# Kernel optimization log

Measured on AMD Instinct MI355X. Metric: run time of the kernel, lower is better.

The kernel has to match this reference:

```python
import jax, jax.numpy as jnp
import numpy as np

B, S, D, H = 2, 2048, 1024, 16
DK = D // H  # 64
THETA = 10000.0


def _rope_tables(max_seq_len, d_k, theta):
    dim_idx = jnp.arange(0, d_k // 2, dtype=jnp.float32)
    freqs = 1.0 / theta ** (2.0 * dim_idx / d_k)
    pos = jnp.arange(0, max_seq_len, dtype=jnp.float32)
    ang = jnp.outer(pos, freqs)  # [S, d_k//2]
    return jnp.sin(ang), jnp.cos(ang)


def setup_inputs() -> dict:
    key = jax.random.key(0)
    ks = jax.random.split(key, 5)
    scale = 0.02
    x = jax.random.normal(ks[0], (B, S, D), dtype=jnp.float32)
    w_q = jax.random.normal(ks[1], (D, D), dtype=jnp.float32) * scale
    w_k = jax.random.normal(ks[2], (D, D), dtype=jnp.float32) * scale
    w_v = jax.random.normal(ks[3], (D, D), dtype=jnp.float32) * scale
    w_o = jax.random.normal(ks[4], (D, D), dtype=jnp.float32) * scale
    sin_tab, cos_tab = _rope_tables(S, DK, THETA)
    token_positions = jnp.broadcast_to(jnp.arange(S, dtype=jnp.int32), (B, S))
    return {"x": x, "w_q": w_q, "w_k": w_k, "w_v": w_v, "w_o": w_o,
            "sin_tab": sin_tab, "cos_tab": cos_tab,
            "token_positions": token_positions}


def _apply_rope(t, sin, cos):
    # t: [B, H, S, DK]; sin/cos: [B, 1, S, DK//2]
    t_even = t[..., 0::2]
    t_odd = t[..., 1::2]
    r_even = cos * t_even - sin * t_odd
    r_odd = sin * t_even + cos * t_odd
    # re-interleave even/odd back into last dim
    out = jnp.stack([r_even, r_odd], axis=-1)  # [B,H,S,DK//2,2]
    return out.reshape(t.shape)


def reference(x, w_q, w_k, w_v, w_o, sin_tab, cos_tab, token_positions):
    b, s, d = x.shape
    q = (x @ w_q.T).reshape(b, s, H, DK).transpose(0, 2, 1, 3)  # [B,H,S,DK]
    k = (x @ w_k.T).reshape(b, s, H, DK).transpose(0, 2, 1, 3)
    v = (x @ w_v.T).reshape(b, s, H, DK).transpose(0, 2, 1, 3)

    sin = sin_tab[token_positions][:, None, :, :]  # [B,1,S,DK//2]
    cos = cos_tab[token_positions][:, None, :, :]
    q = _apply_rope(q, sin, cos)
    k = _apply_rope(k, sin, cos)

    scores = jnp.einsum('bhqd,bhkd->bhqk', q, k) / jnp.sqrt(jnp.float32(DK))
    causal = jnp.tril(jnp.ones((s, s), dtype=bool))  # keep lower triangle
    scores = jnp.where(causal, scores, -jnp.inf)
    probs = jax.nn.softmax(scores, axis=-1)
    attn = jnp.einsum('bhqk,bhkd->bhqd', probs, v)
    attn = attn.transpose(0, 2, 1, 3).reshape(b, s, d)
    return attn @ w_o.T
```

## Files before the change

### kernel.cpp

```cpp
#include <hip/hip_runtime.h>
#include <hip/hip_bf16.h>
#include <cstdint>

#define B_ 2
#define S_ 2048
#define D_ 1024
#define H_ 16
#define DK_ 64
#define HALF_ 32

typedef short bf16x8 __attribute__((ext_vector_type(8)));
typedef float f32x4  __attribute__((ext_vector_type(4)));
typedef unsigned int u32;

static __device__ __forceinline__ unsigned short bfbits(float f) {
    __hip_bfloat16 h = __float2bfloat16(f);
    unsigned short u; __builtin_memcpy(&u, &h, 2); return u;
}
static __device__ __forceinline__ unsigned pack2bf(float a, float b) {
    return (unsigned)bfbits(a) | ((unsigned)bfbits(b) << 16);
}

static __device__ __forceinline__ void gload_lds16(const void* g, void* l) {
    __builtin_amdgcn_global_load_lds(
        (const __attribute__((address_space(1))) u32*)(uintptr_t)g,
        (__attribute__((address_space(3))) u32*)(uintptr_t)l,
        16, 0, 0);
}

__global__ __launch_bounds__(256) void to_bf16_kernel(
    const float* __restrict__ x,
    const float* __restrict__ wq, const float* __restrict__ wk,
    const float* __restrict__ wv, const float* __restrict__ wo,
    const float* __restrict__ sin_tab, const float* __restrict__ cos_tab,
    __hip_bfloat16* __restrict__ xb,
    __hip_bfloat16* __restrict__ wqb, __hip_bfloat16* __restrict__ wkb,
    __hip_bfloat16* __restrict__ wvb, __hip_bfloat16* __restrict__ wob,
    float2* __restrict__ sctab)
{
    const int seg = blockIdx.y;
    if (seg == 8) {
        if (blockIdx.x >= 64) return;
        size_t i = ((size_t)blockIdx.x * 256 + threadIdx.x) * 4;
        float4 c = *reinterpret_cast<const float4*>(cos_tab + i);
        float4 s = *reinterpret_cast<const float4*>(sin_tab + i);
        float4* dst = reinterpret_cast<float4*>(sctab + i);
        dst[0] = make_float4(c.x, s.x, c.y, s.y);
        dst[1] = make_float4(c.z, s.z, c.w, s.w);
        return;
    }
    const float* src;
    __hip_bfloat16* dst;
    size_t off = 0;
    if (seg < 4)       { src = x;  dst = xb;  off = (size_t)seg << 20; }
    else if (seg == 4) { src = wq; dst = wqb; }
    else if (seg == 5) { src = wk; dst = wkb; }
    else if (seg == 6) { src = wv; dst = wvb; }
    else               { src = wo; dst = wob; }
    size_t i = off + ((size_t)blockIdx.x * 256 + threadIdx.x) * 4;
    float4 v = *reinterpret_cast<const float4*>(src + i);
    ushort4 u = make_ushort4(bfbits(v.x), bfbits(v.y), bfbits(v.z), bfbits(v.w));
    *reinterpret_cast<ushort4*>(dst + i) = u;
}

template<int MODE>
__global__ __launch_bounds__(256) void mfma_gemm_kernel(
    const __hip_bfloat16* __restrict__ A,
    const __hip_bfloat16* __restrict__ Wq, const __hip_bfloat16* __restrict__ Wk,
    const __hip_bfloat16* __restrict__ Wv,
    __hip_bfloat16* __restrict__ out_q, __hip_bfloat16* __restrict__ out_k,
    __hip_bfloat16* __restrict__ out_v,
    float* __restrict__ out_f32,
    const float2* __restrict__ sctab,
    const int* __restrict__ tpos)
{
    constexpr int K = 1024;
    const int which = (MODE == 0) ? blockIdx.z : 3;
    const __hip_bfloat16* __restrict__ W =
        (MODE == 1) ? Wq : (which == 0 ? Wq : which == 1 ? Wk : Wv);

    __shared__ __align__(16) unsigned char As[2][128 * 4 * 16];
    __shared__ __align__(16) unsigned char Bs[2][128 * 4 * 16];

    const int tid = threadIdx.x;
    const int wid = tid >> 6;
    const int l   = tid & 63;
    const int g   = l >> 4;
    const int i16 = l & 15;
    const int wr  = wid >> 1, wc = wid & 1;

    const int wg   = blockIdx.x;
    const int tile = (wg & 7) * 32 + (wg >> 3);
    const int row0 = (tile >> 3) * 128;
    const int col0 = (tile & 7) * 128;

    const __hip_bfloat16* Abase = A + (size_t)row0 * K;
    const __hip_bfloat16* Wbase = W + (size_t)col0 * K;

    f32x4 acc[4][4];
    const f32x4 zero = {0.f, 0.f, 0.f, 0.f};
    #pragma unroll
    for (int mi = 0; mi < 4; ++mi)
        #pragma unroll
        for (int ni = 0; ni < 4; ++ni) acc[mi][ni] = zero;

    int a_off[4], b_off[4];
    #pragma unroll
    for (int f = 0; f < 4; ++f) {
        int ra = wr * 64 + f * 16 + i16;
        a_off[f] = (ra * 4 + (g ^ ((ra >> 1) & 3))) * 16;
        int rb = wc * 64 + f * 16 + i16;
        b_off[f] = (rb * 4 + (g ^ ((rb >> 1) & 3))) * 16;
    }

    int st_goff[2], st_loff[2];
    #pragma unroll
    for (int it = 0; it < 2; ++it) {
        int c = it * 256 + wid * 64 + l;
        int row = c >> 2;
        int kc = (c & 3) ^ ((row >> 1) & 3);
        st_goff[it] = row * K + kc * 8;
        st_loff[it] = (it * 256 + wid * 64) * 16;
    }

    #pragma unroll
    for (int it = 0; it < 2; ++it) {
        gload_lds16(Abase + st_goff[it], &As[0][0] + st_loff[it]);
        gload_lds16(Wbase + st_goff[it], &Bs[0][0] + st_loff[it]);
    }
    __syncthreads();

    for (int t = 0; t < K / 32; ++t) {
        const int cur = t & 1;
        if (t + 1 < K / 32) {
            const int k1 = (t + 1) * 32;
            #pragma unroll
            for (int it = 0; it < 2; ++it) {
                gload_lds16(Abase + k1 + st_goff[it], &As[cur ^ 1][0] + st_loff[it]);
                gload_lds16(Wbase + k1 + st_goff[it], &Bs[cur ^ 1][0] + st_loff[it]);
            }
        }
        bf16x8 af[4], bfr[4];
        #pragma unroll
        for (int f = 0; f < 4; ++f) {
            af[f]  = *reinterpret_cast<const bf16x8*>(&As[cur][0] + a_off[f]);
            bfr[f] = *reinterpret_cast<const bf16x8*>(&Bs[cur][0] + b_off[f]);
        }
        #pragma unroll
        for (int mi = 0; mi < 4; ++mi)
            #pragma unroll
            for (int ni = 0; ni < 4; ++ni)
                acc[mi][ni] = __builtin_amdgcn_mfma_f32_16x16x32_bf16(
                    af[mi], bfr[ni], acc[mi][ni], 0, 0, 0);
        __syncthreads();
    }

    if (MODE == 0) {
        __hip_bfloat16* __restrict__ outp =
            which == 0 ? out_q : which == 1 ? out_k : out_v;
        const int head = (col0 >> 6) + wc;
        #pragma unroll
        for (int mi = 0; mi < 4; ++mi) {
            #pragma unroll
            for (int r = 0; r < 4; ++r) {
                const int gi = row0 + wr * 64 + mi * 16 + g * 4 + r;
                const int b_ = gi >> 11;
                const int s_ = gi & (S_ - 1);
                const int pos = tpos[gi];
                const float2* sc = sctab + pos * HALF_;
                __hip_bfloat16* orow =
                    outp + (((size_t)b_ * H_ + head) * S_ + s_) * DK_;
                #pragma unroll
                for (int ni = 0; ni < 4; ++ni) {
                    float val = acc[mi][ni][r];
                    float other = __shfl_xor(val, 1, 64);
                    const int dk = ni * 16 + i16;
                    float res;
                    if (which < 2) {
                        float2 cs = sc[ni * 8 + (i16 >> 1)];
                        res = (i16 & 1) ? fmaf(cs.y, other, cs.x * val)
                                        : (cs.x * val - cs.y * other);
                    } else {
                        res = val;
                    }
                    if (which == 0) res *= 0.180336880f;
                    orow[dk] = __float2bfloat16(res);
                }
            }
        }
    } else {
        #pragma unroll
        for (int mi = 0; mi < 4; ++mi) {
            #pragma unroll
            for (int r = 0; r < 4; ++r) {
                const int gi = row0 + wr * 64 + mi * 16 + g * 4 + r;
                float* orow = out_f32 + (size_t)gi * D_ + col0 + wc * 64;
                #pragma unroll
                for (int ni = 0; ni < 4; ++ni)
                    orow[ni * 16 + i16] = acc[mi][ni][r];
            }
        }
    }
}

__global__ __launch_bounds__(256) void flash_mfma_kernel(
    const __hip_bfloat16* __restrict__ q,
    const __hip_bfloat16* __restrict__ k,
    const __hip_bfloat16* __restrict__ v,
    __hip_bfloat16* __restrict__ attn)
{
    __shared__ __align__(16) unsigned char Ks[2][64 * 128];
    __shared__ __align__(16) unsigned char Vt[2][64 * 128];
    __shared__ __align__(16) unsigned char Ps[4][16 * 128];

    const int tid = threadIdx.x;
    const int w   = tid >> 6;
    const int l   = tid & 63;
    const int g   = l >> 4;
    const int i16 = l & 15;

    const int wgid = blockIdx.x;
    const int xcd  = wgid & 7;
    const int idx  = wgid >> 3;
    const int r_   = idx >> 5;
    const int c_   = idx & 31;
    const int bh   = xcd * 4 + r_;
    const int qsb  = (r_ & 1) ? c_ : (31 - c_);

    const size_t base = (size_t)bh * S_ * DK_;
    const __hip_bfloat16* kb_ = k + base;
    const __hip_bfloat16* vb_ = v + base;
    const int nt = qsb + 1;

    int ksrc[2], kdst[2];
    #pragma unroll
    for (int it = 0; it < 2; ++it) {
        int c = it * 256 + tid;
        int krow = c >> 3;
        int kchunk = (c & 7) ^ (krow & 7);
        ksrc[it] = krow * DK_ + kchunk * 8;
        kdst[it] = c * 16;
    }
    const int vd8_0 = w;
    const int vd8_1 = 4 + w;
    unsigned char* const pw = &Ps[w][0];

    const int qrow = qsb * 64 + w * 16 + i16;

    bf16x8 qf0, qf1;
    {
        const __hip_bfloat16* qp = q + base + (size_t)qrow * DK_ + g * 8;
        qf0 = *reinterpret_cast<const bf16x8*>(qp);
        qf1 = *reinterpret_cast<const bf16x8*>(qp + 32);
    }

    f32x4 o[4] = {};
    float m_run = -1e30f, l_run = 0.0f;

    #pragma unroll
    for (int it = 0; it < 2; ++it)
        gload_lds16(kb_ + ksrc[it], &Ks[0][0] + kdst[it]);
    {
        float4 vv0 = *reinterpret_cast<const float4*>(vb_ + l * DK_ + vd8_0 * 8);
        float4 vv1 = *reinterpret_cast<const float4*>(vb_ + l * DK_ + vd8_1 * 8);
        const unsigned short* u0 = reinterpret_cast<const unsigned short*>(&vv0);
        const unsigned short* u1 = reinterpret_cast<const unsigned short*>(&vv1);
        #pragma unroll
        for (int s = 0; s < 8; ++s) {
            int d0 = vd8_0 * 8 + s;
            *reinterpret_cast<unsigned short*>(&Vt[0][0] + d0 * 128 +
                (((l >> 3) ^ (d0 & 7)) << 4) + (l & 7) * 2) = u0[s];
            int d1 = vd8_1 * 8 + s;
            *reinterpret_cast<unsigned short*>(&Vt[0][0] + d1 * 128 +
                (((l >> 3) ^ (d1 & 7)) << 4) + (l & 7) * 2) = u1[s];
        }
    }
    __syncthreads();

    for (int t = 0; t < nt; ++t) {
        const int cur = t & 1;
        const bool pre = (t + 1 < nt);
        float4 vv0, vv1;
        if (pre) {
            const size_t toff = (size_t)(t + 1) * 64 * DK_;
            #pragma unroll
            for (int it = 0; it < 2; ++it)
                gload_lds16(kb_ + toff + ksrc[it], &Ks[cur ^ 1][0] + kdst[it]);
            vv0 = *reinterpret_cast<const float4*>(vb_ + toff + l * DK_ + vd8_0 * 8);
            vv1 = *reinterpret_cast<const float4*>(vb_ + toff + l * DK_ + vd8_1 * 8);
        }

        f32x4 s_acc[4] = {};
        __builtin_amdgcn_s_setprio(1);
        #pragma unroll
        for (int jf = 0; jf < 4; ++jf) {
            int row = jf * 16 + i16;
            bf16x8 ak0 = *reinterpret_cast<const bf16x8*>(
                &Ks[cur][0] + row * 128 + ((g ^ (row & 7)) << 4));
            s_acc[jf] = __builtin_amdgcn_mfma_f32_16x16x32_bf16(
                ak0, qf0, s_acc[jf], 0, 0, 0);
            bf16x8 ak1 = *reinterpret_cast<const bf16x8*>(
                &Ks[cur][0] + row * 128 + (((4 + g) ^ (row & 7)) << 4));
            s_acc[jf] = __builtin_amdgcn_mfma_f32_16x16x32_bf16(
                ak1, qf1, s_acc[jf], 0, 0, 0);
        }
        __builtin_amdgcn_s_setprio(0);

        if (t == nt - 1) {
            #pragma unroll
            for (int jf = 0; jf < 4; ++jf)
                #pragma unroll
                for (int r = 0; r < 4; ++r)
                    if (t * 64 + jf * 16 + g * 4 + r > qrow)
                        s_acc[jf][r] = -1e30f;
        }

        float mx0 = fmaxf(fmaxf(s_acc[0][0], s_acc[0][1]),
                          fmaxf(s_acc[0][2], s_acc[0][3]));
        float mx1 = fmaxf(fmaxf(s_acc[1][0], s_acc[1][1]),
                          fmaxf(s_acc[1][2], s_acc[1][3]));
        float mx2 = fmaxf(fmaxf(s_acc[2][0], s_acc[2][1]),
                          fmaxf(s_acc[2][2], s_acc[2][3]));
        float mx3 = fmaxf(fmaxf(s_acc[3][0], s_acc[3][1]),
                          fmaxf(s_acc[3][2], s_acc[3][3]));
        float vmax = fmaxf(fmaxf(mx0, mx1), fmaxf(mx2, mx3));

        if (!__all(vmax <= m_run + 11.5f)) {
            float rmax = fmaxf(vmax, __shfl_xor(vmax, 16, 64));
            rmax = fmaxf(rmax, __shfl_xor(rmax, 32, 64));
            float m_new = fmaxf(m_run, rmax);
            float factor = __builtin_amdgcn_exp2f(m_run - m_new);
            m_run = m_new;
            l_run *= factor;
            #pragma unroll
            for (int df = 0; df < 4; ++df)
                #pragma unroll
                for (int r = 0; r < 4; ++r)
                    o[df][r] *= factor;
        }

        float p[4][4];
        float psum = 0.0f;
        #pragma unroll
        for (int jf = 0; jf < 4; ++jf)
            #pragma unroll
            for (int r = 0; r < 4; ++r) {
                p[jf][r] = __builtin_amdgcn_exp2f(s_acc[jf][r] - m_run);
                psum += p[jf][r];
            }
        l_run += psum;

        #pragma unroll
        for (int jf = 0; jf < 4; ++jf)
            #pragma unroll
            for (int r0 = 0; r0 < 4; r0 += 2) {
                unsigned pk = pack2bf(p[jf][r0], p[jf][r0 + 1]);
                int jj = jf * 16 + g * 4 + r0;
                *reinterpret_cast<unsigned*>(pw + i16 * 128 +
                    ((jj * 2) ^ ((i16 & 7) << 4))) = pk;
            }

        __builtin_amdgcn_s_setprio(1);
        #pragma unroll
        for (int jc = 0; jc < 2; ++jc) {
            bf16x8 bp = *reinterpret_cast<const bf16x8*>(pw + i16 * 128 +
                (((jc * 4 + g) ^ (i16 & 7)) << 4));
            #pragma unroll
            for (int df = 0; df < 4; ++df) {
                int row = df * 16 + i16;
                bf16x8 av = *reinterpret_cast<const bf16x8*>(
                    &Vt[cur][0] + row * 128 +
                    (((jc * 4 + g) ^ (row & 7)) << 4));
                o[df] = __builtin_amdgcn_mfma_f32_16x16x32_bf16(
                    av, bp, o[df], 0, 0, 0);
            }
        }
        __builtin_amdgcn_s_setprio(0);

        if (pre) {
            unsigned char* vtb = &Vt[cur ^ 1][0];
            const unsigned short* u0 = reinterpret_cast<const unsigned short*>(&vv0);
            const unsigned short* u1 = reinterpret_cast<const unsigned short*>(&vv1);
            #pragma unroll
            for (int s = 0; s < 8; ++s) {
                int d0 = vd8_0 * 8 + s;
                *reinterpret_cast<unsigned short*>(vtb + d0 * 128 +
                    (((l >> 3) ^ (d0 & 7)) << 4) + (l & 7) * 2) = u0[s];
                int d1 = vd8_1 * 8 + s;
                *reinterpret_cast<unsigned short*>(vtb + d1 * 128 +
                    (((l >> 3) ^ (d1 & 7)) << 4) + (l & 7) * 2) = u1[s];
            }
        }
        __syncthreads();
    }

    float l_tot = l_run;
    l_tot += __shfl_xor(l_tot, 16, 64);
    l_tot += __shfl_xor(l_tot, 32, 64);
    const float inv_l = 1.0f / l_tot;
    const int b_ = bh >> 4, h_ = bh & 15;
    __hip_bfloat16* orow = attn + ((size_t)b_ * S_ + qrow) * D_ + h_ * 64;
    #pragma unroll
    for (int df = 0; df < 4; ++df) {
        ushort4 uo = make_ushort4(
            bfbits(o[df][0] * inv_l), bfbits(o[df][1] * inv_l),
            bfbits(o[df][2] * inv_l), bfbits(o[df][3] * inv_l));
        *reinterpret_cast<ushort4*>(orow + df * 16 + g * 4) = uo;
    }
}

extern "C" void kernel_launch(void* const* d_in, const int* in_sizes, int n_in,
                              void* d_out, int out_size, void* d_ws, size_t ws_size,
                              hipStream_t stream) {
    const float* x       = (const float*)d_in[0];
    const float* w_q     = (const float*)d_in[1];
    const float* w_k     = (const float*)d_in[2];
    const float* w_v     = (const float*)d_in[3];
    const float* w_o     = (const float*)d_in[4];
    const float* sin_tab = (const float*)d_in[5];
    const float* cos_tab = (const float*)d_in[6];
    const int*   tpos    = (const int*)d_in[7];
    float* out = (float*)d_out;

    const size_t nM  = (size_t)B_ * S_ * D_;
    const size_t nW  = (size_t)D_ * D_;
    __hip_bfloat16* xb   = (__hip_bfloat16*)d_ws;
    __hip_bfloat16* wqb  = xb  + nM;
    __hip_bfloat16* wkb  = wqb + nW;
    __hip_bfloat16* wvb  = wkb + nW;
    __hip_bfloat16* wob  = wvb + nW;
    __hip_bfloat16* q_ws = wob + nW;
    __hip_bfloat16* k_ws = q_ws + nM;
    __hip_bfloat16* v_ws = k_ws + nM;
    __hip_bfloat16* a_ws = v_ws + nM;
    float2*         sct  = (float2*)(a_ws + nM);

    to_bf16_kernel<<<dim3(1024, 9), 256, 0, stream>>>(
        x, w_q, w_k, w_v, w_o, sin_tab, cos_tab,
        xb, wqb, wkb, wvb, wob, sct);
    mfma_gemm_kernel<0><<<dim3(256, 1, 3), 256, 0, stream>>>(
        xb, wqb, wkb, wvb, q_ws, k_ws, v_ws, nullptr, sct, tpos);
    flash_mfma_kernel<<<1024, 256, 0, stream>>>(
        q_ws, k_ws, v_ws, a_ws);
    mfma_gemm_kernel<1><<<dim3(256, 1, 1), 256, 0, stream>>>(
        a_ws, wob, nullptr, nullptr, nullptr, nullptr, nullptr, out,
        sct, tpos);
}
```

Measured before the change: 122.0 us.

## Use 256x256-tile 8-wave GEMM with interleaved prefetch for QKV projection

Replaces the 128x128-tile QKV projection GEMM with a dedicated 512-thread kernel that computes 256x256 output tiles, with each wave holding a 128x64 accumulator block. It uses 64-wide K steps with XOR-swizzled LDS staging, and splits each step into four quadrants so the next tile's global-to-LDS loads interleave with the MFMA work. MFMA sections are bracketed by s_setprio. The goal is more reuse per loaded byte and better overlap of loads with compute. In exchange, each block uses much more LDS (128 KB) and more registers, and the grid shrinks to 192 blocks, which may underfill the 256 CUs.

```diff
diff --git a/kernel.cpp b/kernel.cpp
--- a/kernel.cpp
+++ b/kernel.cpp
@@ -63,21 +63,161 @@
     *reinterpret_cast<ushort4*>(dst + i) = u;
 }
 
-template<int MODE>
-__global__ __launch_bounds__(256) void mfma_gemm_kernel(
+__global__ __launch_bounds__(512) void qkv_gemm8_kernel(
     const __hip_bfloat16* __restrict__ A,
     const __hip_bfloat16* __restrict__ Wq, const __hip_bfloat16* __restrict__ Wk,
     const __hip_bfloat16* __restrict__ Wv,
     __hip_bfloat16* __restrict__ out_q, __hip_bfloat16* __restrict__ out_k,
     __hip_bfloat16* __restrict__ out_v,
-    float* __restrict__ out_f32,
     const float2* __restrict__ sctab,
     const int* __restrict__ tpos)
 {
+    constexpr int K  = 1024;
+    constexpr int NT = K / 64;
+    const int which = blockIdx.z;
+    const __hip_bfloat16* __restrict__ W =
+        which == 0 ? Wq : which == 1 ? Wk : Wv;
+    __hip_bfloat16* __restrict__ outp =
+        which == 0 ? out_q : which == 1 ? out_k : out_v;
+
+    __shared__ __align__(16) unsigned char As[2][32768];
+    __shared__ __align__(16) unsigned char Bs[2][32768];
+
+    const int tid = threadIdx.x;
+    const int w   = tid >> 6;
+    const int l   = tid & 63;
+    const int g   = l >> 4;
+    const int i16 = l & 15;
+    const int wr  = w >> 2;
+    const int wc  = w & 3;
+
+    const int bid = blockIdx.x;
+    const int rt  = (bid & 7) + ((bid >> 3) & 1) * 8;
+    const int ct  = bid >> 4;
+    const int row0 = rt * 256, col0 = ct * 256;
+
+    const __hip_bfloat16* Abase = A + (size_t)row0 * K;
+    const __hip_bfloat16* Wbase = W + (size_t)col0 * K;
+
+    int st_goff[2], st_loff[2];
+    #pragma unroll
+    for (int it = 0; it < 2; ++it) {
+        int c  = it * 512 + tid;
+        int rw = c >> 3;
+        int kc = (c & 7) ^ (rw & 7);
+        st_goff[it] = rw * K + kc * 8;
+        st_loff[it] = c * 16;
+    }
+
+    const int x7 = (i16 & 7) << 4;
+    const int ck0 = (g << 4) ^ x7;
+    const int ck1 = ((4 + g) << 4) ^ x7;
+    int arow[8], brow[4];
+    #pragma unroll
+    for (int mf = 0; mf < 8; ++mf) arow[mf] = (wr * 128 + mf * 16 + i16) * 128;
+    #pragma unroll
+    for (int nf = 0; nf < 4; ++nf) brow[nf] = (wc * 64 + nf * 16 + i16) * 128;
+
+    f32x4 acc[8][4];
+    const f32x4 zero = {0.f, 0.f, 0.f, 0.f};
+    #pragma unroll
+    for (int mf = 0; mf < 8; ++mf)
+        #pragma unroll
+        for (int nf = 0; nf < 4; ++nf) acc[mf][nf] = zero;
+
+    auto STAGE = [&](int isB, int h, int kt, int bufb) {
+        const __hip_bfloat16* gb = isB ? Wbase : Abase;
+        unsigned char* lb = (isB ? &Bs[bufb][0] : &As[bufb][0]) + h * 16384;
+        const size_t go = (size_t)(h * 128) * K + (size_t)kt * 64;
+        #pragma unroll
+        for (int it = 0; it < 2; ++it)
+            gload_lds16(gb + go + st_goff[it], lb + st_loff[it]);
+    };
+
+    auto QUAD = [&](int mh, int nh, int buf) {
+        bf16x8 af[4][2], bfv[2][2];
+        #pragma unroll
+        for (int mi = 0; mi < 4; ++mi) {
+            af[mi][0] = *reinterpret_cast<const bf16x8*>(
+                &As[buf][0] + arow[mh * 4 + mi] + ck0);
+            af[mi][1] = *reinterpret_cast<const bf16x8*>(
+                &As[buf][0] + arow[mh * 4 + mi] + ck1);
+        }
+        #pragma unroll
+        for (int ni = 0; ni < 2; ++ni) {
+            bfv[ni][0] = *reinterpret_cast<const bf16x8*>(
+                &Bs[buf][0] + brow[nh * 2 + ni] + ck0);
+            bfv[ni][1] = *reinterpret_cast<const bf16x8*>(
+                &Bs[buf][0] + brow[nh * 2 + ni] + ck1);
+        }
+        __builtin_amdgcn_s_setprio(1);
+        #pragma unroll
+        for (int mi = 0; mi < 4; ++mi)
+            #pragma unroll
+            for (int ni = 0; ni < 2; ++ni) {
+                acc[mh*4+mi][nh*2+ni] = __builtin_amdgcn_mfma_f32_16x16x32_bf16(
+                    af[mi][0], bfv[ni][0], acc[mh*4+mi][nh*2+ni], 0, 0, 0);
+                acc[mh*4+mi][nh*2+ni] = __builtin_amdgcn_mfma_f32_16x16x32_bf16(
+                    af[mi][1], bfv[ni][1], acc[mh*4+mi][nh*2+ni], 0, 0, 0);
+            }
+        __builtin_amdgcn_s_setprio(0);
+    };
+
+    STAGE(0, 0, 0, 0); STAGE(1, 0, 0, 0); STAGE(0, 1, 0, 0); STAGE(1, 1, 0, 0);
+
+    for (int T = 0; T < NT; ++T) {
+        const int buf = T & 1, nb = buf ^ 1;
+        const bool nl = (T + 1 < NT);
+        asm volatile("s_waitcnt vmcnt(0)\n\ts_barrier" ::: "memory");
+        if (nl) { STAGE(0, 0, T + 1, nb); STAGE(1, 0, T + 1, nb); }
+        QUAD(0, 0, buf);
+        if (nl) STAGE(0, 1, T + 1, nb);
+        QUAD(1, 0, buf);
+        if (nl) STAGE(1, 1, T + 1, nb);
+        QUAD(0, 1, buf);
+        QUAD(1, 1, buf);
+    }
+
+    const int head = ct * 4 + wc;
+    #pragma unroll
+    for (int mf = 0; mf < 8; ++mf) {
+        #pragma unroll
+        for (int r = 0; r < 4; ++r) {
+            const int gi = row0 + wr * 128 + mf * 16 + g * 4 + r;
+            const int b_ = gi >> 11;
+            const int s_ = gi & (S_ - 1);
+            const int pos = tpos[gi];
+            const float2* sc = sctab + pos * HALF_;
+            __hip_bfloat16* orow =
+                outp + (((size_t)b_ * H_ + head) * S_ + s_) * DK_;
+            #pragma unroll
+            for (int nf = 0; nf < 4; ++nf) {
+                float val = acc[mf][nf][r];
+                float other = __shfl_xor(val, 1, 64);
+                const int dk = nf * 16 + i16;
+                float res;
+                if (which < 2) {
+                    float2 cs = sc[nf * 8 + (i16 >> 1)];
+                    res = (i16 & 1) ? fmaf(cs.y, other, cs.x * val)
+                                    : (cs.x * val - cs.y * other);
+                } else {
+                    res = val;
+                }
+                if (which == 0) res *= 0.180336880f;
+                orow[dk] = __float2bfloat16(res);
+            }
+        }
+    }
+}
+
+template<int MODE>
+__global__ __launch_bounds__(256) void mfma_gemm_kernel(
+    const __hip_bfloat16* __restrict__ A,
+    const __hip_bfloat16* __restrict__ Wq,
+    float* __restrict__ out_f32)
+{
     constexpr int K = 1024;
-    const int which = (MODE == 0) ? blockIdx.z : 3;
-    const __hip_bfloat16* __restrict__ W =
-        (MODE == 1) ? Wq : (which == 0 ? Wq : which == 1 ? Wk : Wv);
+    const __hip_bfloat16* __restrict__ W = Wq;
 
     __shared__ __align__(16) unsigned char As[2][128 * 4 * 16];
     __shared__ __align__(16) unsigned char Bs[2][128 * 4 * 16];
@@ -155,50 +295,15 @@
         __syncthreads();
     }
 
-    if (MODE == 0) {
-        __hip_bfloat16* __restrict__ outp =
-            which == 0 ? out_q : which == 1 ? out_k : out_v;
-        const int head = (col0 >> 6) + wc;
-        #pragma unroll
-        for (int mi = 0; mi < 4; ++mi) {
-            #pragma unroll
-            for (int r = 0; r < 4; ++r) {
-                const int gi = row0 + wr * 64 + mi * 16 + g * 4 + r;
-                const int b_ = gi >> 11;
-                const int s_ = gi & (S_ - 1);
-                const int pos = tpos[gi];
-                const float2* sc = sctab + pos * HALF_;
-                __hip_bfloat16* orow =
-                    outp + (((size_t)b_ * H_ + head) * S_ + s_) * DK_;
-                #pragma unroll
-                for (int ni = 0; ni < 4; ++ni) {
-                    float val = acc[mi][ni][r];
-                    float other = __shfl_xor(val, 1, 64);
-                    const int dk = ni * 16 + i16;
-                    float res;
-                    if (which < 2) {
-                        float2 cs = sc[ni * 8 + (i16 >> 1)];
-                        res = (i16 & 1) ? fmaf(cs.y, other, cs.x * val)
-                                        : (cs.x * val - cs.y * other);
-                    } else {
-                        res = val;
-                    }
-                    if (which == 0) res *= 0.180336880f;
-                    orow[dk] = __float2bfloat16(res);
-                }
-            }
-        }
-    } else {
-        #pragma unroll
-        for (int mi = 0; mi < 4; ++mi) {
-            #pragma unroll
-            for (int r = 0; r < 4; ++r) {
-                const int gi = row0 + wr * 64 + mi * 16 + g * 4 + r;
-                float* orow = out_f32 + (size_t)gi * D_ + col0 + wc * 64;
-                #pragma unroll
-                for (int ni = 0; ni < 4; ++ni)
-                    orow[ni * 16 + i16] = acc[mi][ni][r];
-            }
+    #pragma unroll
+    for (int mi = 0; mi < 4; ++mi) {
+        #pragma unroll
+        for (int r = 0; r < 4; ++r) {
+            const int gi = row0 + wr * 64 + mi * 16 + g * 4 + r;
+            float* orow = out_f32 + (size_t)gi * D_ + col0 + wc * 64;
+            #pragma unroll
+            for (int ni = 0; ni < 4; ++ni)
+                orow[ni * 16 + i16] = acc[mi][ni][r];
         }
     }
 }
@@ -438,11 +543,10 @@
     to_bf16_kernel<<<dim3(1024, 9), 256, 0, stream>>>(
         x, w_q, w_k, w_v, w_o, sin_tab, cos_tab,
         xb, wqb, wkb, wvb, wob, sct);
-    mfma_gemm_kernel<0><<<dim3(256, 1, 3), 256, 0, stream>>>(
-        xb, wqb, wkb, wvb, q_ws, k_ws, v_ws, nullptr, sct, tpos);
+    qkv_gemm8_kernel<<<dim3(64, 1, 3), 512, 0, stream>>>(
+        xb, wqb, wkb, wvb, q_ws, k_ws, v_ws, sct, tpos);
     flash_mfma_kernel<<<1024, 256, 0, stream>>>(
         q_ws, k_ws, v_ws, a_ws);
     mfma_gemm_kernel<1><<<dim3(256, 1, 1), 256, 0, stream>>>(
-        a_ws, wob, nullptr, nullptr, nullptr, nullptr, nullptr, out,
-        sct, tpos);
-}
+        a_ws, wob, out);
+}
```

Measured after the change: 134.2 us. +10.1%, slower.

## Triple-buffer K tiles in flash attention with two-ahead async prefetch

Applied to the files above, without the earlier changes.

Adds a third LDS buffer for K. K tiles are now prefetched two iterations ahead with global_load_lds, while V keeps its double buffer. The end-of-iteration __syncthreads is replaced by s_waitcnt vmcnt(2) plus s_barrier, so the newest K prefetch can stay in flight across the barrier. This is meant to hide global-load latency for K, at the cost of 8 KB more shared memory per block, which could lower occupancy.

```diff
diff --git a/kernel.cpp b/kernel.cpp
--- a/kernel.cpp
+++ b/kernel.cpp
@@ -209,7 +209,7 @@
     const __hip_bfloat16* __restrict__ v,
     __hip_bfloat16* __restrict__ attn)
 {
-    __shared__ __align__(16) unsigned char Ks[2][64 * 128];
+    __shared__ __align__(16) unsigned char Ks[3][64 * 128];
     __shared__ __align__(16) unsigned char Vt[2][64 * 128];
     __shared__ __align__(16) unsigned char Ps[4][16 * 128];
 
@@ -260,6 +260,11 @@
     #pragma unroll
     for (int it = 0; it < 2; ++it)
         gload_lds16(kb_ + ksrc[it], &Ks[0][0] + kdst[it]);
+    if (nt > 1) {
+        #pragma unroll
+        for (int it = 0; it < 2; ++it)
+            gload_lds16(kb_ + 64 * DK_ + ksrc[it], &Ks[1][0] + kdst[it]);
+    }
     {
         float4 vv0 = *reinterpret_cast<const float4*>(vb_ + l * DK_ + vd8_0 * 8);
         float4 vv1 = *reinterpret_cast<const float4*>(vb_ + l * DK_ + vd8_1 * 8);
@@ -277,17 +282,24 @@
     }
     __syncthreads();
 
+    int kcur = 0;
+    int kst  = 2;
+
     for (int t = 0; t < nt; ++t) {
-        const int cur = t & 1;
-        const bool pre = (t + 1 < nt);
+        const int vcur = t & 1;
+        const bool preV = (t + 1 < nt);
+        const bool preK = (t + 2 < nt);
         float4 vv0, vv1;
-        if (pre) {
+        if (preV) {
             const size_t toff = (size_t)(t + 1) * 64 * DK_;
-            #pragma unroll
-            for (int it = 0; it < 2; ++it)
-                gload_lds16(kb_ + toff + ksrc[it], &Ks[cur ^ 1][0] + kdst[it]);
             vv0 = *reinterpret_cast<const float4*>(vb_ + toff + l * DK_ + vd8_0 * 8);
             vv1 = *reinterpret_cast<const float4*>(vb_ + toff + l * DK_ + vd8_1 * 8);
+        }
+        if (preK) {
+            const size_t toff = (size_t)(t + 2) * 64 * DK_;
+            #pragma unroll
+            for (int it = 0; it < 2; ++it)
+                gload_lds16(kb_ + toff + ksrc[it], &Ks[kst][0] + kdst[it]);
         }
 
         f32x4 s_acc[4] = {};
@@ -296,11 +308,11 @@
         for (int jf = 0; jf < 4; ++jf) {
             int row = jf * 16 + i16;
             bf16x8 ak0 = *reinterpret_cast<const bf16x8*>(
-                &Ks[cur][0] + row * 128 + ((g ^ (row & 7)) << 4));
+                &Ks[kcur][0] + row * 128 + ((g ^ (row & 7)) << 4));
             s_acc[jf] = __builtin_amdgcn_mfma_f32_16x16x32_bf16(
                 ak0, qf0, s_acc[jf], 0, 0, 0);
             bf16x8 ak1 = *reinterpret_cast<const bf16x8*>(
-                &Ks[cur][0] + row * 128 + (((4 + g) ^ (row & 7)) << 4));
+                &Ks[kcur][0] + row * 128 + (((4 + g) ^ (row & 7)) << 4));
             s_acc[jf] = __builtin_amdgcn_mfma_f32_16x16x32_bf16(
                 ak1, qf1, s_acc[jf], 0, 0, 0);
         }
@@ -369,7 +381,7 @@
             for (int df = 0; df < 4; ++df) {
                 int row = df * 16 + i16;
                 bf16x8 av = *reinterpret_cast<const bf16x8*>(
-                    &Vt[cur][0] + row * 128 +
+                    &Vt[vcur][0] + row * 128 +
                     (((jc * 4 + g) ^ (row & 7)) << 4));
                 o[df] = __builtin_amdgcn_mfma_f32_16x16x32_bf16(
                     av, bp, o[df], 0, 0, 0);
@@ -377,8 +389,8 @@
         }
         __builtin_amdgcn_s_setprio(0);
 
-        if (pre) {
-            unsigned char* vtb = &Vt[cur ^ 1][0];
+        if (preV) {
+            unsigned char* vtb = &Vt[vcur ^ 1][0];
             const unsigned short* u0 = reinterpret_cast<const unsigned short*>(&vv0);
             const unsigned short* u1 = reinterpret_cast<const unsigned short*>(&vv1);
             #pragma unroll
@@ -391,7 +403,11 @@
                     (((l >> 3) ^ (d1 & 7)) << 4) + (l & 7) * 2) = u1[s];
             }
         }
-        __syncthreads();
+        asm volatile("s_waitcnt vmcnt(2) lgkmcnt(0)\n\ts_barrier" ::: "memory");
+        __builtin_amdgcn_sched_barrier(0);
+
+        kcur = (kcur == 2) ? 0 : kcur + 1;
+        kst  = (kst  == 2) ? 0 : kst  + 1;
     }
 
     float l_tot = l_run;
```

After: 134.6 us. 10.4% more time.

## Split long causal query blocks across two workgroups and merge partial softmax results

Applied to the files above, without the earlier changes.

Query blocks 16-31, the ones with the most key tiles, are now each split into two workgroups that cover half the key range. Each half writes unnormalized bf16 partial outputs plus running max and sum to workspace, and a new merge kernel combines them into the attention output. This shortens the longest-running workgroups and evens out load across the 1536 launched workgroups. The cost is an extra kernel launch, extra global traffic for the partials, and bf16 rounding of unnormalized partial outputs.

```diff
diff --git a/kernel.cpp b/kernel.cpp
--- a/kernel.cpp
+++ b/kernel.cpp
@@ -16,6 +16,9 @@
 static __device__ __forceinline__ unsigned short bfbits(float f) {
     __hip_bfloat16 h = __float2bfloat16(f);
     unsigned short u; __builtin_memcpy(&u, &h, 2); return u;
+}
+static __device__ __forceinline__ float bf2f(unsigned short u) {
+    unsigned v = (unsigned)u << 16; float f; __builtin_memcpy(&f, &v, 4); return f;
 }
 static __device__ __forceinline__ unsigned pack2bf(float a, float b) {
     return (unsigned)bfbits(a) | ((unsigned)bfbits(b) << 16);
@@ -207,7 +210,9 @@
     const __hip_bfloat16* __restrict__ q,
     const __hip_bfloat16* __restrict__ k,
     const __hip_bfloat16* __restrict__ v,
-    __hip_bfloat16* __restrict__ attn)
+    __hip_bfloat16* __restrict__ attn,
+    __hip_bfloat16* __restrict__ opart,
+    float2* __restrict__ mlpart)
 {
     __shared__ __align__(16) unsigned char Ks[2][64 * 128];
     __shared__ __align__(16) unsigned char Vt[2][64 * 128];
@@ -222,15 +227,28 @@
     const int wgid = blockIdx.x;
     const int xcd  = wgid & 7;
     const int idx  = wgid >> 3;
-    const int r_   = idx >> 5;
-    const int c_   = idx & 31;
-    const int bh   = xcd * 4 + r_;
-    const int qsb  = (r_ & 1) ? c_ : (31 - c_);
+    const int bh   = xcd * 4 + (idx & 3);
+    const int j    = idx >> 2;
+    int qsb, t0, t1, part;
+    bool split;
+    if (j < 32) {
+        split = true;
+        qsb  = 31 - (j >> 1);
+        part = j & 1;
+        int h = (qsb + 1) >> 1;
+        t0 = part ? h : 0;
+        t1 = part ? (qsb + 1) : h;
+    } else {
+        split = false;
+        qsb  = 47 - j;
+        part = 0;
+        t0 = 0;
+        t1 = qsb + 1;
+    }
 
     const size_t base = (size_t)bh * S_ * DK_;
     const __hip_bfloat16* kb_ = k + base;
     const __hip_bfloat16* vb_ = v + base;
-    const int nt = qsb + 1;
 
     int ksrc[2], kdst[2];
     #pragma unroll
@@ -257,12 +275,13 @@
     f32x4 o[4] = {};
     float m_run = -1e30f, l_run = 0.0f;
 
-    #pragma unroll
-    for (int it = 0; it < 2; ++it)
-        gload_lds16(kb_ + ksrc[it], &Ks[0][0] + kdst[it]);
     {
-        float4 vv0 = *reinterpret_cast<const float4*>(vb_ + l * DK_ + vd8_0 * 8);
-        float4 vv1 = *reinterpret_cast<const float4*>(vb_ + l * DK_ + vd8_1 * 8);
+        const size_t toff = (size_t)t0 * 64 * DK_;
+        #pragma unroll
+        for (int it = 0; it < 2; ++it)
+            gload_lds16(kb_ + toff + ksrc[it], &Ks[0][0] + kdst[it]);
+        float4 vv0 = *reinterpret_cast<const float4*>(vb_ + toff + l * DK_ + vd8_0 * 8);
+        float4 vv1 = *reinterpret_cast<const float4*>(vb_ + toff + l * DK_ + vd8_1 * 8);
         const unsigned short* u0 = reinterpret_cast<const unsigned short*>(&vv0);
         const unsigned short* u1 = reinterpret_cast<const unsigned short*>(&vv1);
         #pragma unroll
@@ -277,9 +296,9 @@
     }
     __syncthreads();
 
-    for (int t = 0; t < nt; ++t) {
-        const int cur = t & 1;
-        const bool pre = (t + 1 < nt);
+    for (int t = t0; t < t1; ++t) {
+        const int cur = (t - t0) & 1;
+        const bool pre = (t + 1 < t1);
         float4 vv0, vv1;
         if (pre) {
             const size_t toff = (size_t)(t + 1) * 64 * DK_;
@@ -306,7 +325,7 @@
         }
         __builtin_amdgcn_s_setprio(0);
 
-        if (t == nt - 1) {
+        if (t == qsb) {
             #pragma unroll
             for (int jf = 0; jf < 4; ++jf)
                 #pragma unroll
@@ -397,16 +416,70 @@
     float l_tot = l_run;
     l_tot += __shfl_xor(l_tot, 16, 64);
     l_tot += __shfl_xor(l_tot, 32, 64);
-    const float inv_l = 1.0f / l_tot;
+
+    if (!split) {
+        const float inv_l = 1.0f / l_tot;
+        const int b_ = bh >> 4, h_ = bh & 15;
+        __hip_bfloat16* orow = attn + ((size_t)b_ * S_ + qrow) * D_ + h_ * 64;
+        #pragma unroll
+        for (int df = 0; df < 4; ++df) {
+            ushort4 uo = make_ushort4(
+                bfbits(o[df][0] * inv_l), bfbits(o[df][1] * inv_l),
+                bfbits(o[df][2] * inv_l), bfbits(o[df][3] * inv_l));
+            *reinterpret_cast<ushort4*>(orow + df * 16 + g * 4) = uo;
+        }
+    } else {
+        const int p_ = (bh * 16 + (qsb - 16)) * 2 + part;
+        const int rloc = w * 16 + i16;
+        if (g == 0) mlpart[p_ * 64 + rloc] = make_float2(m_run, l_tot);
+        __hip_bfloat16* orow = opart + ((size_t)p_ * 64 + rloc) * 64;
+        #pragma unroll
+        for (int df = 0; df < 4; ++df) {
+            ushort4 uo = make_ushort4(
+                bfbits(o[df][0]), bfbits(o[df][1]),
+                bfbits(o[df][2]), bfbits(o[df][3]));
+            *reinterpret_cast<ushort4*>(orow + df * 16 + g * 4) = uo;
+        }
+    }
+}
+
+__global__ __launch_bounds__(256) void merge_kernel(
+    const __hip_bfloat16* __restrict__ opart,
+    const float2* __restrict__ mlpart,
+    __hip_bfloat16* __restrict__ attn)
+{
+    const int u = blockIdx.x * 256 + threadIdx.x;
+    const int row = u >> 4;
+    const int dk0 = (u & 15) * 4;
+    const int bh = row >> 10;
+    const int rem = row & 1023;
+    const int qsb16 = rem >> 6;
+    const int r64 = rem & 63;
+    const int p0 = (bh * 16 + qsb16) * 2;
+
+    float2 ml0 = mlpart[p0 * 64 + r64];
+    float2 ml1 = mlpart[(p0 + 1) * 64 + r64];
+    float mstar = fmaxf(ml0.x, ml1.x);
+    float f0 = __builtin_amdgcn_exp2f(ml0.x - mstar);
+    float f1 = __builtin_amdgcn_exp2f(ml1.x - mstar);
+    float inv = 1.0f / (f0 * ml0.y + f1 * ml1.y);
+
+    ushort4 u0 = *reinterpret_cast<const ushort4*>(
+        opart + ((size_t)p0 * 64 + r64) * 64 + dk0);
+    ushort4 u1 = *reinterpret_cast<const ushort4*>(
+        opart + ((size_t)(p0 + 1) * 64 + r64) * 64 + dk0);
+
+    ushort4 res = make_ushort4(
+        bfbits((f0 * bf2f(u0.x) + f1 * bf2f(u1.x)) * inv),
+        bfbits((f0 * bf2f(u0.y) + f1 * bf2f(u1.y)) * inv),
+        bfbits((f0 * bf2f(u0.z) + f1 * bf2f(u1.z)) * inv),
+        bfbits((f0 * bf2f(u0.w) + f1 * bf2f(u1.w)) * inv));
+
+    const int qsb = 16 + qsb16;
+    const int s_ = qsb * 64 + r64;
     const int b_ = bh >> 4, h_ = bh & 15;
-    __hip_bfloat16* orow = attn + ((size_t)b_ * S_ + qrow) * D_ + h_ * 64;
-    #pragma unroll
-    for (int df = 0; df < 4; ++df) {
-        ushort4 uo = make_ushort4(
-            bfbits(o[df][0] * inv_l), bfbits(o[df][1] * inv_l),
-            bfbits(o[df][2] * inv_l), bfbits(o[df][3] * inv_l));
-        *reinterpret_cast<ushort4*>(orow + df * 16 + g * 4) = uo;
-    }
+    *reinterpret_cast<ushort4*>(
+        attn + ((size_t)b_ * S_ + s_) * D_ + h_ * 64 + dk0) = res;
 }
 
 extern "C" void kernel_launch(void* const* d_in, const int* in_sizes, int n_in,
@@ -434,14 +507,17 @@
     __hip_bfloat16* v_ws = k_ws + nM;
     __hip_bfloat16* a_ws = v_ws + nM;
     float2*         sct  = (float2*)(a_ws + nM);
+    __hip_bfloat16* opart = (__hip_bfloat16*)(sct + 65536);
+    float2*         mlp   = (float2*)(opart + (size_t)1024 * 64 * 64);
 
     to_bf16_kernel<<<dim3(1024, 9), 256, 0, stream>>>(
         x, w_q, w_k, w_v, w_o, sin_tab, cos_tab,
         xb, wqb, wkb, wvb, wob, sct);
     mfma_gemm_kernel<0><<<dim3(256, 1, 3), 256, 0, stream>>>(
         xb, wqb, wkb, wvb, q_ws, k_ws, v_ws, nullptr, sct, tpos);
-    flash_mfma_kernel<<<1024, 256, 0, stream>>>(
-        q_ws, k_ws, v_ws, a_ws);
+    flash_mfma_kernel<<<1536, 256, 0, stream>>>(
+        q_ws, k_ws, v_ws, a_ws, opart, mlp);
+    merge_kernel<<<2048, 256, 0, stream>>>(opart, mlp, a_ws);
     mfma_gemm_kernel<1><<<dim3(256, 1, 1), 256, 0, stream>>>(
         a_ws, wob, nullptr, nullptr, nullptr, nullptr, nullptr, out,
         sct, tpos);
```

Measured after the change: 133.0 us. +9.0%, slower.
